# Kernel tuning notes

Measured on AMD Instinct MI355X. Metric: run time of the kernel, lower is better.

## Reference

```python
import jax, jax.numpy as jnp
import numpy as np

B, H, S, D = 16, 12, 1024, 64  # batch, heads, seq, head_dim (dim=768, num_head=12)


def setup_inputs() -> dict:
    key = jax.random.key(0)
    ks = jax.random.split(key, 9)
    sc = 1.0 / np.sqrt(D)
    return {
        "x": jax.random.normal(ks[0], (B, H, S, D), dtype=jnp.float32),
        "Wq": jax.random.normal(ks[1], (D, D), dtype=jnp.float32) * sc,
        "bq": jax.random.normal(ks[2], (D,), dtype=jnp.float32) * 0.02,
        "Wk": jax.random.normal(ks[3], (D, D), dtype=jnp.float32) * sc,
        "bk": jax.random.normal(ks[4], (D,), dtype=jnp.float32) * 0.02,
        "Wv": jax.random.normal(ks[5], (D, D), dtype=jnp.float32) * sc,
        "bv": jax.random.normal(ks[6], (D,), dtype=jnp.float32) * 0.02,
        "Wo": jax.random.normal(ks[7], (D, D), dtype=jnp.float32) * sc,
        "bo": jax.random.normal(ks[8], (D,), dtype=jnp.float32) * 0.02,
    }


def reference(x, Wq, bq, Wk, bk, Wv, bv, Wo, bo):
    # torch Linear: y = x @ W^T + b, applied to last dim (head_dim)
    q = jnp.einsum("bhsd,ed->bhse", x, Wq) + bq
    k = jnp.einsum("bhsd,ed->bhse", x, Wk) + bk
    v = jnp.einsum("bhsd,ed->bhse", x, Wv) + bv
    scores = jnp.einsum("bhqd,bhkd->bhqk", q, k) / jnp.sqrt(jnp.float32(q.shape[-1]))
    attn = jax.nn.softmax(scores, axis=-1)
    out = jnp.einsum("bhqk,bhkd->bhqd", attn, v)
    out = jnp.einsum("bhsd,ed->bhse", out, Wo) + bo
    return out
```

## Files before the change

kernel.cpp:

```cpp
#include <hip/hip_runtime.h>
#include <math.h>


typedef __bf16 bf16x8 __attribute__((ext_vector_type(8)));
typedef float  f32x4  __attribute__((ext_vector_type(4)));

#define MFMA(a, b, c) __builtin_amdgcn_mfma_f32_16x16x32_bf16((a), (b), (c), 0, 0, 0)

static constexpr int S = 1024;
static constexpr int PAD = 72;
static constexpr float QSCALE = 0.125f * 1.4426950408889634f;

__device__ inline unsigned long long pack4bf(float a, float b, float c, float d) {
    union { __bf16 h[4]; unsigned long long u; } pk;
    pk.h[0] = (__bf16)a; pk.h[1] = (__bf16)b; pk.h[2] = (__bf16)c; pk.h[3] = (__bf16)d;
    return pk.u;
}

union frag_u { bf16x8 v; unsigned long long u[2]; };

__global__ __launch_bounds__(256, 2) void attn(
    const float* __restrict__ x,
    const float* __restrict__ Wq, const float* __restrict__ bq,
    const float* __restrict__ Wk, const float* __restrict__ bk,
    const float* __restrict__ Wv, const float* __restrict__ bv,
    const float* __restrict__ Wo, const float* __restrict__ bo,
    float* __restrict__ out)
{
    __shared__ __align__(16) union {
        __bf16 xq[256][PAD];
        struct {
            __bf16 k[2][64][PAD];
            __bf16 v[2][64][PAD];
        } m;
    } L;
    __shared__ __align__(16) __bf16 lw[2][64][PAD];

    const int tid = threadIdx.x;
    const int w = tid >> 6, lane = tid & 63, m = lane & 15, quad = lane >> 4;
    const int bh = blockIdx.x;
    const int q0 = blockIdx.y * 256 + w * 64;

    const float* xq32 = x + ((size_t)bh * 1024 + blockIdx.y * 256) * 64;
    #pragma unroll
    for (int i = tid * 4; i < 16384; i += 1024) {
        float4 v = *(const float4*)(xq32 + i);
        int r = i >> 6, c = i & 63;
        *(unsigned long long*)&L.xq[r][c] = pack4bf(v.x, v.y, v.z, v.w);
    }
    #pragma unroll
    for (int i = tid * 4; i < 4096; i += 1024) {
        int r = i >> 6, c = i & 63;
        float4 a = *(const float4*)(Wk + i);
        *(unsigned long long*)&lw[0][r][c] = pack4bf(a.x, a.y, a.z, a.w);
        float4 b = *(const float4*)(Wv + i);
        *(unsigned long long*)&lw[1][r][c] = pack4bf(b.x, b.y, b.z, b.w);
    }
    __syncthreads();

    bf16x8 xqf[4][2];
    #pragma unroll
    for (int g = 0; g < 4; g++) {
        xqf[g][0] = *(const bf16x8*)&L.xq[w * 64 + g * 16 + m][quad * 8];
        xqf[g][1] = *(const bf16x8*)&L.xq[w * 64 + g * 16 + m][32 + quad * 8];
    }
    #pragma unroll
    for (int et = 0; et < 4; et++) {
        const float* wqrow = Wq + (size_t)(et * 16 + m) * 64;
        float4 a0 = *(const float4*)(wqrow + quad * 8);
        float4 a1 = *(const float4*)(wqrow + quad * 8 + 4);
        float4 a2 = *(const float4*)(wqrow + 32 + quad * 8);
        float4 a3 = *(const float4*)(wqrow + 36 + quad * 8);
        frag_u wf0, wf1;
        wf0.u[0] = pack4bf(a0.x, a0.y, a0.z, a0.w);
        wf0.u[1] = pack4bf(a1.x, a1.y, a1.z, a1.w);
        wf1.u[0] = pack4bf(a2.x, a2.y, a2.z, a2.w);
        wf1.u[1] = pack4bf(a3.x, a3.y, a3.z, a3.w);
        float4 bias = *(const float4*)(bq + et * 16 + quad * 4);
        #pragma unroll
        for (int g = 0; g < 4; g++) {
            f32x4 acc = {0.f, 0.f, 0.f, 0.f};
            acc = MFMA(wf0.v, xqf[g][0], acc);
            acc = MFMA(wf1.v, xqf[g][1], acc);
            *(unsigned long long*)&L.xq[w * 64 + g * 16 + m][et * 16 + quad * 4] =
                pack4bf((acc[0] + bias.x) * QSCALE, (acc[1] + bias.y) * QSCALE,
                        (acc[2] + bias.z) * QSCALE, (acc[3] + bias.w) * QSCALE);
        }
    }
    bf16x8 qf[4][2];
    #pragma unroll
    for (int g = 0; g < 4; g++) {
        qf[g][0] = *(const bf16x8*)&L.xq[w * 64 + g * 16 + m][quad * 8];
        qf[g][1] = *(const bf16x8*)&L.xq[w * 64 + g * 16 + m][32 + quad * 8];
    }
    __syncthreads();

    float4 bkr[4];
    float  bvr[4];
    #pragma unroll
    for (int et = 0; et < 4; et++) {
        bkr[et] = *(const float4*)(bk + et * 16 + quad * 4);
        bvr[et] = bv[et * 16 + m];
    }

    f32x4 o[4][4];
    float lsum[4] = {0.f, 0.f, 0.f, 0.f};
    #pragma unroll
    for (int g = 0; g < 4; g++)
        #pragma unroll
        for (int n = 0; n < 4; n++) o[g][n] = {0.f, 0.f, 0.f, 0.f};

    const float* xk32 = x + (size_t)bh * 1024 * 64;
    const int p0 = 32 * (w >> 1) + 8 * quad + 4 * (w & 1);

    {
        const float* xrow = xk32 + (size_t)(w * 16 + m) * 64;
        float4 a0 = *(const float4*)(xrow + quad * 8);
        float4 a1 = *(const float4*)(xrow + quad * 8 + 4);
        float4 a2 = *(const float4*)(xrow + 32 + quad * 8);
        float4 a3 = *(const float4*)(xrow + 36 + quad * 8);
        frag_u xk0, xk1;
        xk0.u[0] = pack4bf(a0.x, a0.y, a0.z, a0.w);
        xk0.u[1] = pack4bf(a1.x, a1.y, a1.z, a1.w);
        xk1.u[0] = pack4bf(a2.x, a2.y, a2.z, a2.w);
        xk1.u[1] = pack4bf(a3.x, a3.y, a3.z, a3.w);
        #pragma unroll
        for (int et = 0; et < 4; et++) {
            bf16x8 kw0 = *(const bf16x8*)&lw[0][et * 16 + m][quad * 8];
            bf16x8 kw1 = *(const bf16x8*)&lw[0][et * 16 + m][32 + quad * 8];
            f32x4 ka = {0.f, 0.f, 0.f, 0.f};
            ka = MFMA(kw0, xk0.v, ka);
            ka = MFMA(kw1, xk1.v, ka);
            *(unsigned long long*)&L.m.k[0][w * 16 + m][et * 16 + quad * 4] =
                pack4bf(ka[0] + bkr[et].x, ka[1] + bkr[et].y,
                        ka[2] + bkr[et].z, ka[3] + bkr[et].w);
            bf16x8 vw0 = *(const bf16x8*)&lw[1][et * 16 + m][quad * 8];
            bf16x8 vw1 = *(const bf16x8*)&lw[1][et * 16 + m][32 + quad * 8];
            f32x4 va = {0.f, 0.f, 0.f, 0.f};
            va = MFMA(xk0.v, vw0, va);
            va = MFMA(xk1.v, vw1, va);
            *(unsigned long long*)&L.m.v[0][et * 16 + m][p0] =
                pack4bf(va[0] + bvr[et], va[1] + bvr[et],
                        va[2] + bvr[et], va[3] + bvr[et]);
        }
    }

    for (int kb = 0; kb < 16; kb++) {
        __syncthreads();
        const int cur = kb & 1;

        float4 a0, a1, a2, a3;
        if (kb < 15) {
            const float* xrow = xk32 + (size_t)((kb + 1) * 64 + w * 16 + m) * 64;
            a0 = *(const float4*)(xrow + quad * 8);
            a1 = *(const float4*)(xrow + quad * 8 + 4);
            a2 = *(const float4*)(xrow + 32 + quad * 8);
            a3 = *(const float4*)(xrow + 36 + quad * 8);
        }

        #pragma unroll
        for (int gp = 0; gp < 2; gp++) {
            frag_u pb[2][2];
            #pragma unroll
            for (int t = 0; t < 4; t++) {
                bf16x8 ka0 = *(const bf16x8*)&L.m.k[cur][t * 16 + m][quad * 8];
                bf16x8 ka1 = *(const bf16x8*)&L.m.k[cur][t * 16 + m][32 + quad * 8];
                #pragma unroll
                for (int gl = 0; gl < 2; gl++) {
                    const int g = gp * 2 + gl;
                    f32x4 acc = {0.f, 0.f, 0.f, 0.f};
                    acc = MFMA(ka0, qf[g][0], acc);
                    acc = MFMA(ka1, qf[g][1], acc);
                    float e0 = __builtin_amdgcn_exp2f(acc[0]);
                    float e1 = __builtin_amdgcn_exp2f(acc[1]);
                    float e2 = __builtin_amdgcn_exp2f(acc[2]);
                    float e3 = __builtin_amdgcn_exp2f(acc[3]);
                    lsum[g] += (e0 + e1) + (e2 + e3);
                    pb[gl][t >> 1].u[t & 1] = pack4bf(e0, e1, e2, e3);
                }
            }
            #pragma unroll
            for (int n = 0; n < 4; n++) {
                bf16x8 va0 = *(const bf16x8*)&L.m.v[cur][n * 16 + m][quad * 8];
                bf16x8 va1 = *(const bf16x8*)&L.m.v[cur][n * 16 + m][32 + quad * 8];
                #pragma unroll
                for (int gl = 0; gl < 2; gl++) {
                    const int g = gp * 2 + gl;
                    o[g][n] = MFMA(va0, pb[gl][0].v, o[g][n]);
                    o[g][n] = MFMA(va1, pb[gl][1].v, o[g][n]);
                }
            }
        }

        if (kb < 15) {
            frag_u xk0, xk1;
            xk0.u[0] = pack4bf(a0.x, a0.y, a0.z, a0.w);
            xk0.u[1] = pack4bf(a1.x, a1.y, a1.z, a1.w);
            xk1.u[0] = pack4bf(a2.x, a2.y, a2.z, a2.w);
            xk1.u[1] = pack4bf(a3.x, a3.y, a3.z, a3.w);
            #pragma unroll
            for (int et = 0; et < 4; et++) {
                bf16x8 kw0 = *(const bf16x8*)&lw[0][et * 16 + m][quad * 8];
                bf16x8 kw1 = *(const bf16x8*)&lw[0][et * 16 + m][32 + quad * 8];
                f32x4 ka = {0.f, 0.f, 0.f, 0.f};
                ka = MFMA(kw0, xk0.v, ka);
                ka = MFMA(kw1, xk1.v, ka);
                *(unsigned long long*)&L.m.k[cur ^ 1][w * 16 + m][et * 16 + quad * 4] =
                    pack4bf(ka[0] + bkr[et].x, ka[1] + bkr[et].y,
                            ka[2] + bkr[et].z, ka[3] + bkr[et].w);
                bf16x8 vw0 = *(const bf16x8*)&lw[1][et * 16 + m][quad * 8];
                bf16x8 vw1 = *(const bf16x8*)&lw[1][et * 16 + m][32 + quad * 8];
                f32x4 va = {0.f, 0.f, 0.f, 0.f};
                va = MFMA(xk0.v, vw0, va);
                va = MFMA(xk1.v, vw1, va);
                *(unsigned long long*)&L.m.v[cur ^ 1][et * 16 + m][p0] =
                    pack4bf(va[0] + bvr[et], va[1] + bvr[et],
                            va[2] + bvr[et], va[3] + bvr[et]);
            }
        }
    }

    #pragma unroll
    for (int g = 0; g < 4; g++) {
        lsum[g] += __shfl_xor(lsum[g], 16);
        lsum[g] += __shfl_xor(lsum[g], 32);
    }

    bf16x8 wf[4][2];
    #pragma unroll
    for (int et = 0; et < 4; et++) {
        const float* worow = Wo + (size_t)(et * 16 + m) * 64;
        float4 c0 = *(const float4*)(worow + 4 * quad);
        float4 c1 = *(const float4*)(worow + 16 + 4 * quad);
        float4 c2 = *(const float4*)(worow + 32 + 4 * quad);
        float4 c3 = *(const float4*)(worow + 48 + 4 * quad);
        frag_u f0, f1;
        f0.u[0] = pack4bf(c0.x, c0.y, c0.z, c0.w);
        f0.u[1] = pack4bf(c1.x, c1.y, c1.z, c1.w);
        f1.u[0] = pack4bf(c2.x, c2.y, c2.z, c2.w);
        f1.u[1] = pack4bf(c3.x, c3.y, c3.z, c3.w);
        wf[et][0] = f0.v;
        wf[et][1] = f1.v;
    }
    float biasr[4];
    #pragma unroll
    for (int et = 0; et < 4; et++) biasr[et] = bo[et * 16 + m];

    #pragma unroll
    for (int g = 0; g < 4; g++) {
        const float inv = 1.f / lsum[g];
        frag_u af0, af1;
        af0.u[0] = pack4bf(o[g][0][0] * inv, o[g][0][1] * inv, o[g][0][2] * inv, o[g][0][3] * inv);
        af0.u[1] = pack4bf(o[g][1][0] * inv, o[g][1][1] * inv, o[g][1][2] * inv, o[g][1][3] * inv);
        af1.u[0] = pack4bf(o[g][2][0] * inv, o[g][2][1] * inv, o[g][2][2] * inv, o[g][2][3] * inv);
        af1.u[1] = pack4bf(o[g][3][0] * inv, o[g][3][1] * inv, o[g][3][2] * inv, o[g][3][3] * inv);
        #pragma unroll
        for (int et = 0; et < 4; et++) {
            f32x4 acc = {0.f, 0.f, 0.f, 0.f};
            acc = MFMA(af0.v, wf[et][0], acc);
            acc = MFMA(af1.v, wf[et][1], acc);
            #pragma unroll
            for (int r = 0; r < 4; r++) {
                size_t row = (size_t)bh * S + q0 + g * 16 + quad * 4 + r;
                out[row * 64 + et * 16 + m] = acc[r] + biasr[et];
            }
        }
    }
}

extern "C" void kernel_launch(void* const* d_in, const int* in_sizes, int n_in,
                              void* d_out, int out_size, void* d_ws, size_t ws_size,
                              hipStream_t stream) {
    const float* x  = (const float*)d_in[0];
    const float* Wq = (const float*)d_in[1];
    const float* bq = (const float*)d_in[2];
    const float* Wk = (const float*)d_in[3];
    const float* bk = (const float*)d_in[4];
    const float* Wv = (const float*)d_in[5];
    const float* bv = (const float*)d_in[6];
    const float* Wo = (const float*)d_in[7];
    const float* bo = (const float*)d_in[8];
    float* out = (float*)d_out;

    attn<<<dim3(192, 4), 256, 0, stream>>>(x, Wq, bq, Wk, bk, Wv, bv, Wo, bo, out);
}
```

Measured before the change: 214.6 us.

## Halve query tile per block, raise occupancy, and pre-swizzle K/V weights in LDS

Each block now handles 128 queries instead of 256, doubling the grid to 192x8. Launch bounds rise to 3 blocks per CU, with smaller register and LDS footprints per block. Wk/Wv are stored in LDS in MFMA-fragment order so each lane reads a contiguous 16 bytes, and the main attention loop is wrapped in s_setprio. The cost is that K/V projection work doubles, since each block recomputes K and V for the whole sequence, and less Q reuse per K/V tile.

New measurement: 220.4 us. 1.03x slower.

```diff
diff --git a/kernel.cpp b/kernel.cpp
--- a/kernel.cpp
+++ b/kernel.cpp
@@ -19,7 +19,7 @@
 
 union frag_u { bf16x8 v; unsigned long long u[2]; };
 
-__global__ __launch_bounds__(256, 2) void attn(
+__global__ __launch_bounds__(256, 3) void attn(
     const float* __restrict__ x,
     const float* __restrict__ Wq, const float* __restrict__ bq,
     const float* __restrict__ Wk, const float* __restrict__ bk,
@@ -28,41 +28,45 @@
     float* __restrict__ out)
 {
     __shared__ __align__(16) union {
-        __bf16 xq[256][PAD];
+        __bf16 xq[128][PAD];
         struct {
             __bf16 k[2][64][PAD];
             __bf16 v[2][64][PAD];
         } m;
     } L;
-    __shared__ __align__(16) __bf16 lw[2][64][PAD];
+    __shared__ __align__(16) __bf16 lw[2][8][64][8];
 
     const int tid = threadIdx.x;
     const int w = tid >> 6, lane = tid & 63, m = lane & 15, quad = lane >> 4;
     const int bh = blockIdx.x;
-    const int q0 = blockIdx.y * 256 + w * 64;
-
-    const float* xq32 = x + ((size_t)bh * 1024 + blockIdx.y * 256) * 64;
-    #pragma unroll
-    for (int i = tid * 4; i < 16384; i += 1024) {
+    const int q0 = blockIdx.y * 128 + w * 32;
+
+    const float* xq32 = x + ((size_t)bh * 1024 + blockIdx.y * 128) * 64;
+    #pragma unroll
+    for (int i = tid * 4; i < 8192; i += 1024) {
         float4 v = *(const float4*)(xq32 + i);
         int r = i >> 6, c = i & 63;
         *(unsigned long long*)&L.xq[r][c] = pack4bf(v.x, v.y, v.z, v.w);
     }
     #pragma unroll
-    for (int i = tid * 4; i < 4096; i += 1024) {
-        int r = i >> 6, c = i & 63;
-        float4 a = *(const float4*)(Wk + i);
-        *(unsigned long long*)&lw[0][r][c] = pack4bf(a.x, a.y, a.z, a.w);
-        float4 b = *(const float4*)(Wv + i);
-        *(unsigned long long*)&lw[1][r][c] = pack4bf(b.x, b.y, b.z, b.w);
+    for (int c = tid; c < 1024; c += 256) {
+        int mtx = c >> 9, rest = c & 511;
+        int fe = rest >> 6, ln = rest & 63;
+        int mm = ln & 15, qq = ln >> 4;
+        int et = fe >> 1, half = fe & 1;
+        const float* src = (mtx ? Wv : Wk) + (size_t)(et * 16 + mm) * 64 + half * 32 + qq * 8;
+        float4 u0 = *(const float4*)(src);
+        float4 u1 = *(const float4*)(src + 4);
+        *(unsigned long long*)&lw[mtx][fe][ln][0] = pack4bf(u0.x, u0.y, u0.z, u0.w);
+        *(unsigned long long*)&lw[mtx][fe][ln][4] = pack4bf(u1.x, u1.y, u1.z, u1.w);
     }
     __syncthreads();
 
-    bf16x8 xqf[4][2];
-    #pragma unroll
-    for (int g = 0; g < 4; g++) {
-        xqf[g][0] = *(const bf16x8*)&L.xq[w * 64 + g * 16 + m][quad * 8];
-        xqf[g][1] = *(const bf16x8*)&L.xq[w * 64 + g * 16 + m][32 + quad * 8];
+    bf16x8 xqf[2][2];
+    #pragma unroll
+    for (int g = 0; g < 2; g++) {
+        xqf[g][0] = *(const bf16x8*)&L.xq[w * 32 + g * 16 + m][quad * 8];
+        xqf[g][1] = *(const bf16x8*)&L.xq[w * 32 + g * 16 + m][32 + quad * 8];
     }
     #pragma unroll
     for (int et = 0; et < 4; et++) {
@@ -78,20 +82,20 @@
         wf1.u[1] = pack4bf(a3.x, a3.y, a3.z, a3.w);
         float4 bias = *(const float4*)(bq + et * 16 + quad * 4);
         #pragma unroll
-        for (int g = 0; g < 4; g++) {
+        for (int g = 0; g < 2; g++) {
             f32x4 acc = {0.f, 0.f, 0.f, 0.f};
             acc = MFMA(wf0.v, xqf[g][0], acc);
             acc = MFMA(wf1.v, xqf[g][1], acc);
-            *(unsigned long long*)&L.xq[w * 64 + g * 16 + m][et * 16 + quad * 4] =
+            *(unsigned long long*)&L.xq[w * 32 + g * 16 + m][et * 16 + quad * 4] =
                 pack4bf((acc[0] + bias.x) * QSCALE, (acc[1] + bias.y) * QSCALE,
                         (acc[2] + bias.z) * QSCALE, (acc[3] + bias.w) * QSCALE);
         }
     }
-    bf16x8 qf[4][2];
-    #pragma unroll
-    for (int g = 0; g < 4; g++) {
-        qf[g][0] = *(const bf16x8*)&L.xq[w * 64 + g * 16 + m][quad * 8];
-        qf[g][1] = *(const bf16x8*)&L.xq[w * 64 + g * 16 + m][32 + quad * 8];
+    bf16x8 qf[2][2];
+    #pragma unroll
+    for (int g = 0; g < 2; g++) {
+        qf[g][0] = *(const bf16x8*)&L.xq[w * 32 + g * 16 + m][quad * 8];
+        qf[g][1] = *(const bf16x8*)&L.xq[w * 32 + g * 16 + m][32 + quad * 8];
     }
     __syncthreads();
 
@@ -103,10 +107,10 @@
         bvr[et] = bv[et * 16 + m];
     }
 
-    f32x4 o[4][4];
-    float lsum[4] = {0.f, 0.f, 0.f, 0.f};
-    #pragma unroll
-    for (int g = 0; g < 4; g++)
+    f32x4 o[2][4];
+    float lsum[2] = {0.f, 0.f};
+    #pragma unroll
+    for (int g = 0; g < 2; g++)
         #pragma unroll
         for (int n = 0; n < 4; n++) o[g][n] = {0.f, 0.f, 0.f, 0.f};
 
@@ -126,16 +130,16 @@
         xk1.u[1] = pack4bf(a3.x, a3.y, a3.z, a3.w);
         #pragma unroll
         for (int et = 0; et < 4; et++) {
-            bf16x8 kw0 = *(const bf16x8*)&lw[0][et * 16 + m][quad * 8];
-            bf16x8 kw1 = *(const bf16x8*)&lw[0][et * 16 + m][32 + quad * 8];
+            bf16x8 kw0 = *(const bf16x8*)&lw[0][et * 2 + 0][lane][0];
+            bf16x8 kw1 = *(const bf16x8*)&lw[0][et * 2 + 1][lane][0];
             f32x4 ka = {0.f, 0.f, 0.f, 0.f};
             ka = MFMA(kw0, xk0.v, ka);
             ka = MFMA(kw1, xk1.v, ka);
             *(unsigned long long*)&L.m.k[0][w * 16 + m][et * 16 + quad * 4] =
                 pack4bf(ka[0] + bkr[et].x, ka[1] + bkr[et].y,
                         ka[2] + bkr[et].z, ka[3] + bkr[et].w);
-            bf16x8 vw0 = *(const bf16x8*)&lw[1][et * 16 + m][quad * 8];
-            bf16x8 vw1 = *(const bf16x8*)&lw[1][et * 16 + m][32 + quad * 8];
+            bf16x8 vw0 = *(const bf16x8*)&lw[1][et * 2 + 0][lane][0];
+            bf16x8 vw1 = *(const bf16x8*)&lw[1][et * 2 + 1][lane][0];
             f32x4 va = {0.f, 0.f, 0.f, 0.f};
             va = MFMA(xk0.v, vw0, va);
             va = MFMA(xk1.v, vw1, va);
@@ -158,39 +162,36 @@
             a3 = *(const float4*)(xrow + 36 + quad * 8);
         }
 
-        #pragma unroll
-        for (int gp = 0; gp < 2; gp++) {
-            frag_u pb[2][2];
-            #pragma unroll
-            for (int t = 0; t < 4; t++) {
-                bf16x8 ka0 = *(const bf16x8*)&L.m.k[cur][t * 16 + m][quad * 8];
-                bf16x8 ka1 = *(const bf16x8*)&L.m.k[cur][t * 16 + m][32 + quad * 8];
-                #pragma unroll
-                for (int gl = 0; gl < 2; gl++) {
-                    const int g = gp * 2 + gl;
-                    f32x4 acc = {0.f, 0.f, 0.f, 0.f};
-                    acc = MFMA(ka0, qf[g][0], acc);
-                    acc = MFMA(ka1, qf[g][1], acc);
-                    float e0 = __builtin_amdgcn_exp2f(acc[0]);
-                    float e1 = __builtin_amdgcn_exp2f(acc[1]);
-                    float e2 = __builtin_amdgcn_exp2f(acc[2]);
-                    float e3 = __builtin_amdgcn_exp2f(acc[3]);
-                    lsum[g] += (e0 + e1) + (e2 + e3);
-                    pb[gl][t >> 1].u[t & 1] = pack4bf(e0, e1, e2, e3);
-                }
-            }
-            #pragma unroll
-            for (int n = 0; n < 4; n++) {
-                bf16x8 va0 = *(const bf16x8*)&L.m.v[cur][n * 16 + m][quad * 8];
-                bf16x8 va1 = *(const bf16x8*)&L.m.v[cur][n * 16 + m][32 + quad * 8];
-                #pragma unroll
-                for (int gl = 0; gl < 2; gl++) {
-                    const int g = gp * 2 + gl;
-                    o[g][n] = MFMA(va0, pb[gl][0].v, o[g][n]);
-                    o[g][n] = MFMA(va1, pb[gl][1].v, o[g][n]);
-                }
-            }
-        }
+        __builtin_amdgcn_s_setprio(1);
+        frag_u pb[2][2];
+        #pragma unroll
+        for (int t = 0; t < 4; t++) {
+            bf16x8 ka0 = *(const bf16x8*)&L.m.k[cur][t * 16 + m][quad * 8];
+            bf16x8 ka1 = *(const bf16x8*)&L.m.k[cur][t * 16 + m][32 + quad * 8];
+            #pragma unroll
+            for (int g = 0; g < 2; g++) {
+                f32x4 acc = {0.f, 0.f, 0.f, 0.f};
+                acc = MFMA(ka0, qf[g][0], acc);
+                acc = MFMA(ka1, qf[g][1], acc);
+                float e0 = __builtin_amdgcn_exp2f(acc[0]);
+                float e1 = __builtin_amdgcn_exp2f(acc[1]);
+                float e2 = __builtin_amdgcn_exp2f(acc[2]);
+                float e3 = __builtin_amdgcn_exp2f(acc[3]);
+                lsum[g] += (e0 + e1) + (e2 + e3);
+                pb[g][t >> 1].u[t & 1] = pack4bf(e0, e1, e2, e3);
+            }
+        }
+        #pragma unroll
+        for (int n = 0; n < 4; n++) {
+            bf16x8 va0 = *(const bf16x8*)&L.m.v[cur][n * 16 + m][quad * 8];
+            bf16x8 va1 = *(const bf16x8*)&L.m.v[cur][n * 16 + m][32 + quad * 8];
+            #pragma unroll
+            for (int g = 0; g < 2; g++) {
+                o[g][n] = MFMA(va0, pb[g][0].v, o[g][n]);
+                o[g][n] = MFMA(va1, pb[g][1].v, o[g][n]);
+            }
+        }
+        __builtin_amdgcn_s_setprio(0);
 
         if (kb < 15) {
             frag_u xk0, xk1;
@@ -200,16 +201,16 @@
             xk1.u[1] = pack4bf(a3.x, a3.y, a3.z, a3.w);
             #pragma unroll
             for (int et = 0; et < 4; et++) {
-                bf16x8 kw0 = *(const bf16x8*)&lw[0][et * 16 + m][quad * 8];
-                bf16x8 kw1 = *(const bf16x8*)&lw[0][et * 16 + m][32 + quad * 8];
+                bf16x8 kw0 = *(const bf16x8*)&lw[0][et * 2 + 0][lane][0];
+                bf16x8 kw1 = *(const bf16x8*)&lw[0][et * 2 + 1][lane][0];
                 f32x4 ka = {0.f, 0.f, 0.f, 0.f};
                 ka = MFMA(kw0, xk0.v, ka);
                 ka = MFMA(kw1, xk1.v, ka);
                 *(unsigned long long*)&L.m.k[cur ^ 1][w * 16 + m][et * 16 + quad * 4] =
                     pack4bf(ka[0] + bkr[et].x, ka[1] + bkr[et].y,
                             ka[2] + bkr[et].z, ka[3] + bkr[et].w);
-                bf16x8 vw0 = *(const bf16x8*)&lw[1][et * 16 + m][quad * 8];
-                bf16x8 vw1 = *(const bf16x8*)&lw[1][et * 16 + m][32 + quad * 8];
+                bf16x8 vw0 = *(const bf16x8*)&lw[1][et * 2 + 0][lane][0];
+                bf16x8 vw1 = *(const bf16x8*)&lw[1][et * 2 + 1][lane][0];
                 f32x4 va = {0.f, 0.f, 0.f, 0.f};
                 va = MFMA(xk0.v, vw0, va);
                 va = MFMA(xk1.v, vw1, va);
@@ -221,7 +222,7 @@
     }
 
     #pragma unroll
-    for (int g = 0; g < 4; g++) {
+    for (int g = 0; g < 2; g++) {
         lsum[g] += __shfl_xor(lsum[g], 16);
         lsum[g] += __shfl_xor(lsum[g], 32);
     }
@@ -247,7 +248,7 @@
     for (int et = 0; et < 4; et++) biasr[et] = bo[et * 16 + m];
 
     #pragma unroll
-    for (int g = 0; g < 4; g++) {
+    for (int g = 0; g < 2; g++) {
         const float inv = 1.f / lsum[g];
         frag_u af0, af1;
         af0.u[0] = pack4bf(o[g][0][0] * inv, o[g][0][1] * inv, o[g][0][2] * inv, o[g][0][3] * inv);
@@ -282,5 +283,5 @@
     const float* bo = (const float*)d_in[8];
     float* out = (float*)d_out;
 
-    attn<<<dim3(192, 4), 256, 0, stream>>>(x, Wq, bq, Wk, bk, Wv, bv, Wo, bo, out);
+    attn<<<dim3(192, 8), 256, 0, stream>>>(x, Wq, bq, Wk, bk, Wv, bv, Wo, bo, out);
 }
```

## Shrink weight LDS to fragment-major layout, raise occupancy to 3, add setprio

Applied to the files above, without the earlier changes.

Stores the Wk/Wv bf16 weights in shared memory pre-arranged in MFMA fragment order (unpadded), so each lane reads one contiguous 16-byte chunk and the LDS footprint drops. Raises the launch-bounds occupancy target from 2 to 3 blocks per CU, which lowers the register cap per thread. Raises wave priority around the QK/softmax/PV MFMA section so compute waves get issued ahead of the projection phase. Forcing the tighter register budget risks spills in a kernel that holds many accumulators.

New measurement: 287.3 us. 33.9% more time.

```diff
diff --git a/kernel.cpp b/kernel.cpp
--- a/kernel.cpp
+++ b/kernel.cpp
@@ -19,7 +19,7 @@
 
 union frag_u { bf16x8 v; unsigned long long u[2]; };
 
-__global__ __launch_bounds__(256, 2) void attn(
+__global__ __launch_bounds__(256, 3) void attn(
     const float* __restrict__ x,
     const float* __restrict__ Wq, const float* __restrict__ bq,
     const float* __restrict__ Wk, const float* __restrict__ bk,
@@ -34,7 +34,7 @@
             __bf16 v[2][64][PAD];
         } m;
     } L;
-    __shared__ __align__(16) __bf16 lw[2][64][PAD];
+    __shared__ __align__(16) __bf16 lw[2][8][64][8];
 
     const int tid = threadIdx.x;
     const int w = tid >> 6, lane = tid & 63, m = lane & 15, quad = lane >> 4;
@@ -49,12 +49,16 @@
         *(unsigned long long*)&L.xq[r][c] = pack4bf(v.x, v.y, v.z, v.w);
     }
     #pragma unroll
-    for (int i = tid * 4; i < 4096; i += 1024) {
-        int r = i >> 6, c = i & 63;
-        float4 a = *(const float4*)(Wk + i);
-        *(unsigned long long*)&lw[0][r][c] = pack4bf(a.x, a.y, a.z, a.w);
-        float4 b = *(const float4*)(Wv + i);
-        *(unsigned long long*)&lw[1][r][c] = pack4bf(b.x, b.y, b.z, b.w);
+    for (int c = tid; c < 1024; c += 256) {
+        int mtx = c >> 9, rest = c & 511;
+        int fe = rest >> 6, ln = rest & 63;
+        int mm = ln & 15, qq = ln >> 4;
+        int et = fe >> 1, half = fe & 1;
+        const float* src = (mtx ? Wv : Wk) + (size_t)(et * 16 + mm) * 64 + half * 32 + qq * 8;
+        float4 u0 = *(const float4*)(src);
+        float4 u1 = *(const float4*)(src + 4);
+        *(unsigned long long*)&lw[mtx][fe][ln][0] = pack4bf(u0.x, u0.y, u0.z, u0.w);
+        *(unsigned long long*)&lw[mtx][fe][ln][4] = pack4bf(u1.x, u1.y, u1.z, u1.w);
     }
     __syncthreads();
 
@@ -126,16 +130,16 @@
         xk1.u[1] = pack4bf(a3.x, a3.y, a3.z, a3.w);
         #pragma unroll
         for (int et = 0; et < 4; et++) {
-            bf16x8 kw0 = *(const bf16x8*)&lw[0][et * 16 + m][quad * 8];
-            bf16x8 kw1 = *(const bf16x8*)&lw[0][et * 16 + m][32 + quad * 8];
+            bf16x8 kw0 = *(const bf16x8*)&lw[0][et * 2 + 0][lane][0];
+            bf16x8 kw1 = *(const bf16x8*)&lw[0][et * 2 + 1][lane][0];
             f32x4 ka = {0.f, 0.f, 0.f, 0.f};
             ka = MFMA(kw0, xk0.v, ka);
             ka = MFMA(kw1, xk1.v, ka);
             *(unsigned long long*)&L.m.k[0][w * 16 + m][et * 16 + quad * 4] =
                 pack4bf(ka[0] + bkr[et].x, ka[1] + bkr[et].y,
                         ka[2] + bkr[et].z, ka[3] + bkr[et].w);
-            bf16x8 vw0 = *(const bf16x8*)&lw[1][et * 16 + m][quad * 8];
-            bf16x8 vw1 = *(const bf16x8*)&lw[1][et * 16 + m][32 + quad * 8];
+            bf16x8 vw0 = *(const bf16x8*)&lw[1][et * 2 + 0][lane][0];
+            bf16x8 vw1 = *(const bf16x8*)&lw[1][et * 2 + 1][lane][0];
             f32x4 va = {0.f, 0.f, 0.f, 0.f};
             va = MFMA(xk0.v, vw0, va);
             va = MFMA(xk1.v, vw1, va);
@@ -158,6 +162,7 @@
             a3 = *(const float4*)(xrow + 36 + quad * 8);
         }
 
+        __builtin_amdgcn_s_setprio(1);
         #pragma unroll
         for (int gp = 0; gp < 2; gp++) {
             frag_u pb[2][2];
@@ -191,6 +196,7 @@
                 }
             }
         }
+        __builtin_amdgcn_s_setprio(0);
 
         if (kb < 15) {
             frag_u xk0, xk1;
@@ -200,16 +206,16 @@
             xk1.u[1] = pack4bf(a3.x, a3.y, a3.z, a3.w);
             #pragma unroll
             for (int et = 0; et < 4; et++) {
-                bf16x8 kw0 = *(const bf16x8*)&lw[0][et * 16 + m][quad * 8];
-                bf16x8 kw1 = *(const bf16x8*)&lw[0][et * 16 + m][32 + quad * 8];
+                bf16x8 kw0 = *(const bf16x8*)&lw[0][et * 2 + 0][lane][0];
+                bf16x8 kw1 = *(const bf16x8*)&lw[0][et * 2 + 1][lane][0];
                 f32x4 ka = {0.f, 0.f, 0.f, 0.f};
                 ka = MFMA(kw0, xk0.v, ka);
                 ka = MFMA(kw1, xk1.v, ka);
                 *(unsigned long long*)&L.m.k[cur ^ 1][w * 16 + m][et * 16 + quad * 4] =
                     pack4bf(ka[0] + bkr[et].x, ka[1] + bkr[et].y,
                             ka[2] + bkr[et].z, ka[3] + bkr[et].w);
-                bf16x8 vw0 = *(const bf16x8*)&lw[1][et * 16 + m][quad * 8];
-                bf16x8 vw1 = *(const bf16x8*)&lw[1][et * 16 + m][32 + quad * 8];
+                bf16x8 vw0 = *(const bf16x8*)&lw[1][et * 2 + 0][lane][0];
+                bf16x8 vw1 = *(const bf16x8*)&lw[1][et * 2 + 1][lane][0];
                 f32x4 va = {0.f, 0.f, 0.f, 0.f};
                 va = MFMA(xk0.v, vw0, va);
                 va = MFMA(xk1.v, vw1, va);
```
